# Kernel tuning notes

Measured on AMD Instinct MI355X. Metric: run time of the kernel, lower is better.

Reference implementation:

```python
import jax, jax.numpy as jnp
import numpy as np

INSIZE = 512
OUTSIZE = 512
N_U = 64
N_V = 64
SIGMA_MIN = 0.1
SIGMA_MAX = 1.0
BATCH = 8192


def setup_inputs() -> dict:
    key = jax.random.key(0)
    kx, kp, ku, kv, kb = jax.random.split(key, 5)
    x = jax.random.normal(kx, (BATCH, INSIZE), dtype=jnp.float32)
    nsigma = min(INSIZE, OUTSIZE)
    p = 0.001 * jax.random.normal(kp, (nsigma,), dtype=jnp.float32)
    U = jnp.triu(jax.random.normal(ku, (INSIZE, INSIZE), dtype=jnp.float32))
    V = jnp.triu(jax.random.normal(kv, (OUTSIZE, OUTSIZE), dtype=jnp.float32))
    bound = 1.0 / float(np.sqrt(INSIZE))
    bias = jax.random.uniform(kb, (1, OUTSIZE), minval=-bound, maxval=bound, dtype=jnp.float32)
    return {"x": x, "p": p, "U": U, "V": V, "bias": bias}


def _house_chain(x, rows):
    # Sequentially apply Householder reflections. rows[i] has its leading
    # entries zeroed (upper-triangular structure), which makes the full-width
    # dot/outer-product exactly equal to torch's Hprod on the trailing slice
    # u[-k:] while leaving the leading columns of x untouched.
    def step(x, u):
        alpha = 2.0 * (x @ u) / jnp.dot(u, u)  # [B]
        return x - alpha[:, None] * u[None, :], None
    x, _ = jax.lax.scan(step, x, rows)
    return x


def _sigma_matrix(p, dtype):
    r = (SIGMA_MAX - SIGMA_MIN) / 2.0
    sigma_mean = SIGMA_MIN + r
    sigmas = 2.0 * r * (jax.nn.sigmoid(p) - 0.5) + sigma_mean  # [nsigma]
    nsigma = min(INSIZE, OUTSIZE)
    idx = jnp.arange(nsigma)
    return jnp.zeros((INSIZE, OUTSIZE), dtype=dtype).at[idx, idx].set(sigmas.astype(dtype))


def reference(x, p, U, V, bias):
    # Umultiply: i = 0 .. N_U-1, reflector U[i] with k = insize - i
    x = _house_chain(x, jnp.triu(U)[:N_U])
    # x @ Sigma (rectangular diagonal of constrained singular values)
    x = x @ _sigma_matrix(p, x.dtype)
    # Vmultiply: i = N_V-1 down to 0, reflector V[i] with k = outsize - i
    x = _house_chain(x, jnp.triu(V)[:N_V][::-1])
    return x + bias
```

## Files before the change

### kernel.cpp

```cpp
#include <hip/hip_runtime.h>
#include <hip/hip_bf16.h>
#include <math.h>


#define INSIZE 512
#define NREF 64
#define BATCH 8192

static constexpr int OFF_WT    = 0;
static constexpr int OFF_SIGMA = 131072;
static constexpr int OFF_BETAU = OFF_SIGMA + 512;
static constexpr int OFF_BETAV = OFF_BETAU + 64;
static constexpr int OFF_GU    = OFF_BETAV + 64;
static constexpr int OFF_GV    = OFF_GU + 4096;
static constexpr int OFF_C     = OFF_GV + 4096;
static constexpr int OFF_PT    = OFF_C + 4096;
static constexpr int OFF_R     = OFF_PT + 128 * 512;

__device__ inline float sigma_of(float pv) {
    float s = 1.0f / (1.0f + expf(-pv));
    return 0.55f + 0.9f * (s - 0.5f);
}

__global__ __launch_bounds__(256) void k_prep(const float* __restrict__ U,
                                              const float* __restrict__ V,
                                              const float* __restrict__ p,
                                              float* __restrict__ ws) {
    int b = blockIdx.x, t = threadIdx.x;
    if (b == 192) {
        for (int c = t; c < INSIZE; c += 256)
            (ws + OFF_SIGMA)[c] = sigma_of(p[c]);
        return;
    }
    __shared__ float rowi[INSIZE];
    int w = t >> 6, l = t & 63;
    if (b < 128) {
        bool isV = (b >= 64);
        int i = isV ? (b - 64) : b;
        const float* src = isV ? V : U;
        int srow = isV ? (63 - i) : i;
        for (int c = t; c < INSIZE; c += 256) rowi[c] = src[srow * INSIZE + c];
        __syncthreads();
        float* G = ws + (isV ? OFF_GV : OFF_GU);
        float* beta = ws + (isV ? OFF_BETAV : OFF_BETAU);
        for (int jj = 0; jj < 16; ++jj) {
            int j = w * 16 + jj;
            int jrow = isV ? (63 - j) : j;
            const float* rj = src + jrow * INSIZE;
            float s = 0.f;
            for (int c = l; c < INSIZE; c += 64) s += rowi[c] * rj[c];
            for (int o = 32; o > 0; o >>= 1) s += __shfl_down(s, o, 64);
            if (l == 0) {
                G[i * 64 + j] = s;
                if (j == i) beta[i] = 2.0f / s;
            }
        }
    } else {
        int i = b - 128;
        for (int c = t; c < INSIZE; c += 256)
            rowi[c] = U[i * INSIZE + c] * sigma_of(p[c]);
        __syncthreads();
        float* C = ws + OFF_C;
        for (int jj = 0; jj < 16; ++jj) {
            int j = w * 16 + jj;
            const float* rj = V + (63 - j) * INSIZE;
            float s = 0.f;
            for (int c = l; c < INSIZE; c += 64) s += rowi[c] * rj[c];
            for (int o = 32; o > 0; o >>= 1) s += __shfl_down(s, o, 64);
            if (l == 0) C[i * 64 + j] = s;
        }
    }
}

__global__ __launch_bounds__(512) void k_AR(const float* __restrict__ U,
                                            const float* __restrict__ V,
                                            float* __restrict__ ws) {
    __shared__ float Gs[64 * 64];
    __shared__ float bs[64];
    int z = blockIdx.x;
    int t = threadIdx.x;
    const float* G = ws + (z ? OFF_GV : OFF_GU);
    const float* beta = ws + (z ? OFF_BETAV : OFF_BETAU);
    for (int i = t; i < 4096; i += 512) Gs[i] = G[i];
    if (t < 64) bs[t] = beta[t];
    __syncthreads();
    float acc[64];
    if (z == 0) {
        float* At = ws + OFF_PT;
#pragma unroll
        for (int j = 0; j < 64; ++j) {
            float s = U[j * INSIZE + t];
#pragma unroll
            for (int m = 0; m < j; ++m) s -= acc[m] * Gs[m * 64 + j];
            acc[j] = s * bs[j];
        }
#pragma unroll
        for (int j = 0; j < 64; ++j) At[j * INSIZE + t] = acc[j];
    } else {
        float* R = ws + OFF_R;
#pragma unroll
        for (int i = 63; i >= 0; --i) {
            float s = V[(63 - i) * INSIZE + t];
#pragma unroll
            for (int m = i + 1; m < 64; ++m) s -= Gs[i * 64 + m] * acc[m];
            acc[i] = s * bs[i];
        }
#pragma unroll
        for (int i = 0; i < 64; ++i) R[i * INSIZE + t] = acc[i];
    }
}

__global__ __launch_bounds__(256) void k_E(const float* __restrict__ V,
                                           float* __restrict__ ws) {
    int b = blockIdx.x, t = threadIdx.x;
    int j = (b & 15) * 4 + (t >> 6);
    int r = (b >> 4) * 64 + (t & 63);
    const float* At = ws + OFF_PT;
    const float* C = ws + OFF_C;
    float e = (ws + OFF_SIGMA)[r] * V[(63 - j) * INSIZE + r];
#pragma unroll 8
    for (int i = 0; i < 64; ++i)
        e -= At[i * INSIZE + r] * C[i * 64 + j];
    (ws + OFF_PT)[(64 + j) * INSIZE + r] = e;
}

__global__ __launch_bounds__(256) void k_Wt(const float* __restrict__ U,
                                            float* __restrict__ ws) {
    __shared__ float Ps[128][34];
    __shared__ float Qs[128][34];
    int t = threadIdx.x;
    int r0 = (blockIdx.x >> 4) * 32;
    int c0 = (blockIdx.x & 15) * 32;
    const float* PT = ws + OFF_PT;
    const float* R = ws + OFF_R;
    const float* sig = ws + OFF_SIGMA;
    int lr = t & 31, kb = t >> 5;
    float sc = sig[c0 + lr];
#pragma unroll
    for (int ii = 0; ii < 16; ++ii) {
        int k = kb + ii * 8;
        Ps[k][lr] = PT[k * INSIZE + r0 + lr];
        Qs[k][lr] = (k < 64) ? U[k * INSIZE + c0 + lr] * sc
                             : R[(k - 64) * INSIZE + c0 + lr];
    }
    __syncthreads();
    int ty = t >> 4, tx = t & 15;
    float a00 = 0.f, a01 = 0.f, a10 = 0.f, a11 = 0.f;
#pragma unroll
    for (int k = 0; k < 128; ++k) {
        float2 a = *(const float2*)&Ps[k][ty * 2];
        float2 bq = *(const float2*)&Qs[k][tx * 2];
        a00 += a.x * bq.x; a01 += a.x * bq.y;
        a10 += a.y * bq.x; a11 += a.y * bq.y;
    }
    int rg = r0 + ty * 2, cg = c0 + tx * 2;
    float w00 = ((rg == cg) ? sig[rg] : 0.f) - a00;
    float w01 = ((rg == cg + 1) ? sig[rg] : 0.f) - a01;
    float w10 = ((rg + 1 == cg) ? sig[rg + 1] : 0.f) - a10;
    float w11 = ((rg + 1 == cg + 1) ? sig[rg + 1] : 0.f) - a11;
    unsigned short* Wt = (unsigned short*)(ws + OFF_WT);
    __hip_bfloat162 lo = __float22bfloat162_rn(make_float2(w00, w10));
    __hip_bfloat162 hi = __float22bfloat162_rn(make_float2(w01, w11));
    *(__hip_bfloat162*)&Wt[cg * INSIZE + rg] = lo;
    *(__hip_bfloat162*)&Wt[(cg + 1) * INSIZE + rg] = hi;
}

typedef __attribute__((ext_vector_type(8))) short short8;
typedef __attribute__((ext_vector_type(4))) float float4v;

__global__ __launch_bounds__(256) void k_gemm(const float* __restrict__ X,
                                              const float* __restrict__ ws,
                                              const float* __restrict__ bias,
                                              float* __restrict__ out) {
    __shared__ float As[128 * 32];
    __shared__ unsigned short Bs[128 * 32];
    const unsigned short* Wt = (const unsigned short*)(ws + OFF_WT);

    int L = blockIdx.x;
    int jj = L >> 3, x = L & 7;
    int bn = jj & 3;
    int bm = (jj >> 2) * 8 + x;
    int row0 = bm * 128, col0 = bn * 128;

    int t = threadIdx.x;
    int l = t & 63, w = t >> 6;
    int wm = (w >> 1) * 64, wn = (w & 1) * 64;

    float4v acc[4][4] = {};
    int quad = l >> 4;
    int lan = l & 15;

    for (int k0 = 0; k0 < INSIZE; k0 += 32) {
        __syncthreads();
#pragma unroll
        for (int i = 0; i < 4; ++i) {
            int P = i * 256 + t;
            int prow = P >> 3, pc = P & 7;
            int lc = pc ^ (prow & 7);
            const float* g = X + (size_t)(row0 + prow) * INSIZE + k0 + lc * 4;
            __builtin_amdgcn_global_load_lds(
                (const __attribute__((address_space(1))) void*)g,
                (__attribute__((address_space(3))) void*)(As + P * 4), 16, 0, 0);
        }
#pragma unroll
        for (int i = 0; i < 2; ++i) {
            int P = i * 256 + t;
            int prow = P >> 2, pc = P & 3;
            int lc = pc ^ ((prow >> 1) & 3);
            const unsigned short* g = Wt + (size_t)(col0 + prow) * INSIZE + k0 + lc * 8;
            __builtin_amdgcn_global_load_lds(
                (const __attribute__((address_space(1))) void*)g,
                (__attribute__((address_space(3))) void*)(Bs + P * 8), 16, 0, 0);
        }
        __syncthreads();

        short8 af[4];
        short8 bf[4];
#pragma unroll
        for (int mi = 0; mi < 4; ++mi) {
            int rl = wm + mi * 16 + lan;
            int c0q = quad * 2;
            const float4v lo = *(const float4v*)(As + (rl * 8 + (c0q ^ (rl & 7))) * 4);
            const float4v hi = *(const float4v*)(As + (rl * 8 + ((c0q + 1) ^ (rl & 7))) * 4);
            union { short8 s; __hip_bfloat162 h[4]; } u;
            u.h[0] = __float22bfloat162_rn(make_float2(lo[0], lo[1]));
            u.h[1] = __float22bfloat162_rn(make_float2(lo[2], lo[3]));
            u.h[2] = __float22bfloat162_rn(make_float2(hi[0], hi[1]));
            u.h[3] = __float22bfloat162_rn(make_float2(hi[2], hi[3]));
            af[mi] = u.s;
        }
#pragma unroll
        for (int ni = 0; ni < 4; ++ni) {
            int rn = wn + ni * 16 + lan;
            int c = quad ^ ((rn >> 1) & 3);
            bf[ni] = *(const short8*)(Bs + (rn * 4 + c) * 8);
        }
#pragma unroll
        for (int mi = 0; mi < 4; ++mi)
#pragma unroll
            for (int ni = 0; ni < 4; ++ni)
                acc[mi][ni] = __builtin_amdgcn_mfma_f32_16x16x32_bf16(
                    af[mi], bf[ni], acc[mi][ni], 0, 0, 0);
    }

#pragma unroll
    for (int ni = 0; ni < 4; ++ni) {
        int c = col0 + wn + ni * 16 + lan;
        float bv = bias[c];
#pragma unroll
        for (int mi = 0; mi < 4; ++mi) {
            int rbase = row0 + wm + mi * 16 + quad * 4;
#pragma unroll
            for (int r = 0; r < 4; ++r)
                out[(size_t)(rbase + r) * INSIZE + c] = acc[mi][ni][r] + bv;
        }
    }
}

extern "C" void kernel_launch(void* const* d_in, const int* in_sizes, int n_in,
                              void* d_out, int out_size, void* d_ws, size_t ws_size,
                              hipStream_t stream) {
    const float* x    = (const float*)d_in[0];
    const float* p    = (const float*)d_in[1];
    const float* U    = (const float*)d_in[2];
    const float* V    = (const float*)d_in[3];
    const float* bias = (const float*)d_in[4];
    float* ws  = (float*)d_ws;
    float* out = (float*)d_out;

    k_prep<<<193, 256, 0, stream>>>(U, V, p, ws);
    k_AR<<<2, 512, 0, stream>>>(U, V, ws);
    k_E<<<128, 256, 0, stream>>>(V, ws);
    k_Wt<<<256, 256, 0, stream>>>(U, ws);
    k_gemm<<<256, 256, 0, stream>>>(x, ws, bias, out);
}
```

Baseline: 136.3 us.

## Fuse E computation into Wt kernel and halve GEMM M-tile to 64 rows

Merges the k_E kernel into the Wt-building kernel. Each block now computes its slice of the E rows in shared memory from the staged A and C tiles instead of writing them to and rereading them from global memory, which removes one launch. This recomputes E redundantly across the 16 column blocks. Separately, the main GEMM tile shrinks from 128x128 to 64x128, giving 512 blocks instead of 256 for better CU occupancy on the 8192x512x512 problem, at the cost of less reuse of W per block.

```diff
diff --git a/kernel.cpp b/kernel.cpp
--- a/kernel.cpp
+++ b/kernel.cpp
@@ -110,38 +110,43 @@
     }
 }
 
-__global__ __launch_bounds__(256) void k_E(const float* __restrict__ V,
-                                           float* __restrict__ ws) {
-    int b = blockIdx.x, t = threadIdx.x;
-    int j = (b & 15) * 4 + (t >> 6);
-    int r = (b >> 4) * 64 + (t & 63);
-    const float* At = ws + OFF_PT;
-    const float* C = ws + OFF_C;
-    float e = (ws + OFF_SIGMA)[r] * V[(63 - j) * INSIZE + r];
-#pragma unroll 8
-    for (int i = 0; i < 64; ++i)
-        e -= At[i * INSIZE + r] * C[i * 64 + j];
-    (ws + OFF_PT)[(64 + j) * INSIZE + r] = e;
-}
-
-__global__ __launch_bounds__(256) void k_Wt(const float* __restrict__ U,
-                                            float* __restrict__ ws) {
+__global__ __launch_bounds__(256) void k_WtE(const float* __restrict__ U,
+                                             const float* __restrict__ V,
+                                             float* __restrict__ ws) {
     __shared__ float Ps[128][34];
     __shared__ float Qs[128][34];
+    __shared__ float Cs[4096];
     int t = threadIdx.x;
     int r0 = (blockIdx.x >> 4) * 32;
     int c0 = (blockIdx.x & 15) * 32;
-    const float* PT = ws + OFF_PT;
+    const float* At = ws + OFF_PT;
     const float* R = ws + OFF_R;
     const float* sig = ws + OFF_SIGMA;
     int lr = t & 31, kb = t >> 5;
     float sc = sig[c0 + lr];
 #pragma unroll
+    for (int ii = 0; ii < 8; ++ii) {
+        int k = kb + ii * 8;
+        Ps[k][lr] = At[k * INSIZE + r0 + lr];
+    }
+#pragma unroll
     for (int ii = 0; ii < 16; ++ii) {
         int k = kb + ii * 8;
-        Ps[k][lr] = PT[k * INSIZE + r0 + lr];
         Qs[k][lr] = (k < 64) ? U[k * INSIZE + c0 + lr] * sc
                              : R[(k - 64) * INSIZE + c0 + lr];
+    }
+#pragma unroll
+    for (int i = 0; i < 16; ++i) Cs[t + i * 256] = (ws + OFF_C)[t + i * 256];
+    __syncthreads();
+    float sr = sig[r0 + lr];
+#pragma unroll
+    for (int ii = 0; ii < 8; ++ii) {
+        int j = kb * 8 + ii;
+        float e = sr * V[(63 - j) * INSIZE + r0 + lr];
+#pragma unroll 8
+        for (int i = 0; i < 64; ++i)
+            e -= Ps[i][lr] * Cs[i * 64 + j];
+        Ps[64 + j][lr] = e;
     }
     __syncthreads();
     int ty = t >> 4, tx = t & 15;
@@ -172,28 +177,28 @@
                                               const float* __restrict__ ws,
                                               const float* __restrict__ bias,
                                               float* __restrict__ out) {
-    __shared__ float As[128 * 32];
+    __shared__ float As[64 * 32];
     __shared__ unsigned short Bs[128 * 32];
     const unsigned short* Wt = (const unsigned short*)(ws + OFF_WT);
 
     int L = blockIdx.x;
-    int jj = L >> 3, x = L & 7;
-    int bn = jj & 3;
-    int bm = (jj >> 2) * 8 + x;
-    int row0 = bm * 128, col0 = bn * 128;
+    int inner = L & 7;
+    int bn = (L >> 3) & 3;
+    int bm = (L >> 5) * 8 + inner;
+    int row0 = bm * 64, col0 = bn * 128;
 
     int t = threadIdx.x;
     int l = t & 63, w = t >> 6;
-    int wm = (w >> 1) * 64, wn = (w & 1) * 64;
-
-    float4v acc[4][4] = {};
+    int wm = (w & 1) * 32, wn = (w >> 1) * 64;
+
+    float4v acc[2][4] = {};
     int quad = l >> 4;
     int lan = l & 15;
 
     for (int k0 = 0; k0 < INSIZE; k0 += 32) {
         __syncthreads();
 #pragma unroll
-        for (int i = 0; i < 4; ++i) {
+        for (int i = 0; i < 2; ++i) {
             int P = i * 256 + t;
             int prow = P >> 3, pc = P & 7;
             int lc = pc ^ (prow & 7);
@@ -214,10 +219,10 @@
         }
         __syncthreads();
 
-        short8 af[4];
+        short8 af[2];
         short8 bf[4];
 #pragma unroll
-        for (int mi = 0; mi < 4; ++mi) {
+        for (int mi = 0; mi < 2; ++mi) {
             int rl = wm + mi * 16 + lan;
             int c0q = quad * 2;
             const float4v lo = *(const float4v*)(As + (rl * 8 + (c0q ^ (rl & 7))) * 4);
@@ -236,7 +241,7 @@
             bf[ni] = *(const short8*)(Bs + (rn * 4 + c) * 8);
         }
 #pragma unroll
-        for (int mi = 0; mi < 4; ++mi)
+        for (int mi = 0; mi < 2; ++mi)
 #pragma unroll
             for (int ni = 0; ni < 4; ++ni)
                 acc[mi][ni] = __builtin_amdgcn_mfma_f32_16x16x32_bf16(
@@ -248,7 +253,7 @@
         int c = col0 + wn + ni * 16 + lan;
         float bv = bias[c];
 #pragma unroll
-        for (int mi = 0; mi < 4; ++mi) {
+        for (int mi = 0; mi < 2; ++mi) {
             int rbase = row0 + wm + mi * 16 + quad * 4;
 #pragma unroll
             for (int r = 0; r < 4; ++r)
@@ -270,7 +275,6 @@
 
     k_prep<<<193, 256, 0, stream>>>(U, V, p, ws);
     k_AR<<<2, 512, 0, stream>>>(U, V, ws);
-    k_E<<<128, 256, 0, stream>>>(V, ws);
-    k_Wt<<<256, 256, 0, stream>>>(U, ws);
-    k_gemm<<<256, 256, 0, stream>>>(x, ws, bias, out);
-}
+    k_WtE<<<256, 256, 0, stream>>>(U, V, ws);
+    k_gemm<<<512, 256, 0, stream>>>(x, ws, bias, out);
+}
```

Measured after the change: 130.0 us. 4.6% less time.
